# Optimization experiments

Hardware: AMD Instinct MI355X
Metric: run time of the kernel (lower is better)

## Reference

```python
import jax, jax.numpy as jnp
import numpy as np

SERIES_LEN = 4096
D_EMB = 1024
D_V = 1024
HURST = 0.7
H = HURST - 0.5          # exponent used by the module
DT = 1.0 / SERIES_LEN
EPS = 1e-8


def _attn_matrix():
    # Lower-triangular fractional power-law matrix A2[i, j]:
    #   j <  i : ((i - j) * dt + 1e-8) ** (hurst - 0.5)
    #   j == i : 1e-8 ** (hurst - 0.5)
    #   j >  i : 0
    i = jnp.arange(SERIES_LEN, dtype=jnp.int32)[:, None]
    j = jnp.arange(SERIES_LEN, dtype=jnp.int32)[None, :]
    diff = jnp.clip(i - j, 1, None).astype(jnp.float32)  # safe base for fractional power
    lower = jnp.where(i > j, (diff * DT + EPS) ** H, 0.0)
    diag = jnp.eye(SERIES_LEN, dtype=jnp.float32) * (EPS ** H)
    return lower + diag  # (L, L) float32


def setup_inputs() -> dict:
    key = jax.random.key(0)
    k1, k2 = jax.random.split(key)
    embed_series = jax.random.normal(k1, (D_EMB, SERIES_LEN), dtype=jnp.float32)
    # nn.Linear(d_emb, d_v, bias=False) weight has shape (d_v, d_emb)
    Wv_weight = jax.random.normal(k2, (D_V, D_EMB), dtype=jnp.float32) * (1.0 / np.sqrt(D_EMB))
    return {"embed_series": embed_series, "Wv_weight": Wv_weight}


def reference(embed_series, Wv_weight):
    # V (original, d_v x L) = Wv(embed_series.T).T ; output[i, c] = sum_j A2[i, j] * V[c, j]
    # => out = A2 @ (embed_series.T @ Wv_weight.T), shape (L, d_v)
    A2 = _attn_matrix()                                   # (L, L) lower triangular
    Y = jnp.einsum('el,ve->lv', embed_series, Wv_weight)  # (L, d_v)
    return A2 @ Y                                         # (L, d_v)
```

## Files before the change

kernel.cpp:

```cpp
#include <hip/hip_runtime.h>
#include <hip/hip_bf16.h>
#include <cstdint>
#include <cstddef>


#define L_SER 4096
#define DEMB  1024
#define DV    1024

#define R_STRIDE 4224
#define R_O0     4096
#define LDP      72

typedef __bf16 bf16_t;
typedef __attribute__((ext_vector_type(8))) __bf16 bf16x8;
typedef __attribute__((ext_vector_type(4))) float f32x4;

__global__ void prep_kernel(const float* __restrict__ E, const float* __restrict__ W,
                            bf16_t* __restrict__ Eb, bf16_t* __restrict__ Wb,
                            bf16_t* __restrict__ R) {
    const int b = blockIdx.x;
    if (b < 132) {
        int idx = b * 256 + threadIdx.x;
        int s = idx / R_STRIDE;
        int x = idx - s * R_STRIDE;
        int d = R_O0 + s - x;
        float v = 0.0f;
        if (d >= 0 && d < L_SER)
            v = powf((d == 0) ? 1e-8f : ((float)d * (1.0f / (float)L_SER) + 1e-8f), 0.2f);
        R[idx] = (bf16_t)v;
    } else if (b < 132 + 2048) {
        int idx = (b - 132) * 256 + threadIdx.x;
        const f32x4* s = (const f32x4*)E;
        f32x4 v0 = s[idx * 2], v1 = s[idx * 2 + 1];
        bf16x8 o;
        o[0] = (bf16_t)v0[0]; o[1] = (bf16_t)v0[1]; o[2] = (bf16_t)v0[2]; o[3] = (bf16_t)v0[3];
        o[4] = (bf16_t)v1[0]; o[5] = (bf16_t)v1[1]; o[6] = (bf16_t)v1[2]; o[7] = (bf16_t)v1[3];
        ((bf16x8*)Eb)[idx] = o;
    } else {
        int idx = (b - 2180) * 256 + threadIdx.x;
        const f32x4* s = (const f32x4*)W;
        f32x4 v0 = s[idx * 2], v1 = s[idx * 2 + 1];
        bf16x8 o;
        o[0] = (bf16_t)v0[0]; o[1] = (bf16_t)v0[1]; o[2] = (bf16_t)v0[2]; o[3] = (bf16_t)v0[3];
        o[4] = (bf16_t)v1[0]; o[5] = (bf16_t)v1[1]; o[6] = (bf16_t)v1[2]; o[7] = (bf16_t)v1[3];
        ((bf16x8*)Wb)[idx] = o;
    }
}

#define GA_STAGE(SBOFS, RA, RB)                                              \
    _Pragma("unroll")                                                        \
    for (int c = 0; c < 4; ++c) {                                            \
        *(bf16x8*)&sA[(SBOFS) + (c * 32 + srow) * LDP + kc8] = RA[c];        \
        *(bf16x8*)&sB[(SBOFS) + (c * 32 + srow) * LDP + kc8] = RB[c];        \
    }

#define GA_PREFETCH(RA, RB)                                                  \
    _Pragma("unroll")                                                        \
    for (int c = 0; c < 4; ++c) {                                            \
        RA[c] = *(const bf16x8*)pA[c];                                       \
        RB[c] = *(const bf16x8*)pB[c];                                       \
        pA[c] += 64; pB[c] += 64;                                            \
    }

#define GA_COMPUTE(SBOFS)                                                    \
    _Pragma("unroll")                                                        \
    for (int kk = 0; kk < 2; ++kk) {                                         \
        bf16x8 afr[4], bfr[4];                                               \
        _Pragma("unroll")                                                    \
        for (int tm = 0; tm < 4; ++tm)                                       \
            afr[tm] = *(const bf16x8*)&sA[(SBOFS) + (wm * 64 + tm * 16 + ln) * LDP + kk * 32 + quad * 8]; \
        _Pragma("unroll")                                                    \
        for (int tn = 0; tn < 4; ++tn)                                       \
            bfr[tn] = *(const bf16x8*)&sB[(SBOFS) + (wn * 64 + tn * 16 + ln) * LDP + kk * 32 + quad * 8]; \
        _Pragma("unroll")                                                    \
        for (int tm = 0; tm < 4; ++tm)                                       \
            _Pragma("unroll")                                                \
            for (int tn = 0; tn < 4; ++tn)                                   \
                acc[tm][tn] = __builtin_amdgcn_mfma_f32_16x16x32_bf16(afr[tm], bfr[tn], acc[tm][tn], 0, 0, 0); \
    }

__global__ __launch_bounds__(256, 2) void gemm_a_kernel(const bf16_t* __restrict__ R,
                                                        const bf16_t* __restrict__ Eb,
                                                        bf16_t* __restrict__ T0,
                                                        bf16_t* __restrict__ T1) {
    __shared__ __align__(16) bf16_t sA[2 * 128 * LDP];
    __shared__ __align__(16) bf16_t sB[2 * 128 * LDP];

    const int bid = blockIdx.x;
    int I, nb, h;
    if (bid < 256) { I = bid >> 3;                nb = bid & 7;         h = 0; }
    else           { I = 31 - ((bid - 256) >> 3); nb = (bid - 256) & 7; h = 1; }
    const int i0 = I * 128;
    const int n0 = nb * 128;
    const int nsteps = I + 1;
    const int j0b = h ? 64 * (I + 1) : 0;
    bf16_t* __restrict__ Tout = h ? T1 : T0;

    const int tid  = threadIdx.x;
    const int wave = tid >> 6;
    const int lane = tid & 63;
    const int quad = lane >> 4;
    const int ln   = lane & 15;
    const int wm   = wave >> 1;
    const int wn   = wave & 1;
    const int srow = tid >> 3;
    const int kc8  = (tid & 7) * 8;

    f32x4 acc[4][4];
#pragma unroll
    for (int a = 0; a < 4; ++a)
#pragma unroll
        for (int b = 0; b < 4; ++b) acc[a][b] = (f32x4){0, 0, 0, 0};

    const bf16_t* pA[4];
    const bf16_t* pB[4];
    bf16x8 ra0[4], rb0[4], ra1[4], rb1[4];
#pragma unroll
    for (int c = 0; c < 4; ++c) {
        int r = c * 32 + srow;
        pA[c] = R + (size_t)(r & 7) * R_STRIDE + (R_O0 - i0 + j0b - 8 * (r >> 3) + kc8);
        pB[c] = Eb + (size_t)(n0 + c * 32 + srow) * L_SER + j0b + kc8;
    }
    GA_PREFETCH(ra0, rb0)
    if (nsteps > 1) { GA_PREFETCH(ra1, rb1) }

    for (int s = 0;; s += 2) {
        GA_STAGE(0, ra0, rb0)
        __syncthreads();
        if (s + 2 < nsteps) { GA_PREFETCH(ra0, rb0) }
        GA_COMPUTE(0)
        if (s + 1 >= nsteps) break;
        GA_STAGE(128 * LDP, ra1, rb1)
        __syncthreads();
        if (s + 3 < nsteps) { GA_PREFETCH(ra1, rb1) }
        GA_COMPUTE(128 * LDP)
        if (s + 2 >= nsteps) break;
    }

#pragma unroll
    for (int tm = 0; tm < 4; ++tm) {
        int row_base = i0 + wm * 64 + tm * 16 + quad * 4;
#pragma unroll
        for (int tn = 0; tn < 4; ++tn) {
            int col = n0 + wn * 64 + tn * 16 + ln;
#pragma unroll
            for (int r = 0; r < 4; ++r)
                Tout[(size_t)(row_base + r) * DEMB + col] = (bf16_t)acc[tm][tn][r];
        }
    }
}

#define GB_STAGE(SBOFS_A, SBOFS_B, RA, RB)                                   \
    _Pragma("unroll")                                                        \
    for (int c = 0; c < 2; ++c)                                              \
        *(bf16x8*)&sA[(SBOFS_A) + (c * 32 + srow) * LDP + kc8] = RA[c];      \
    _Pragma("unroll")                                                        \
    for (int c = 0; c < 4; ++c)                                              \
        *(bf16x8*)&sB[(SBOFS_B) + (c * 32 + srow) * LDP + kc8] = RB[c];

#define GB_PREFETCH(RA, RB)                                                  \
    _Pragma("unroll")                                                        \
    for (int c = 0; c < 2; ++c) {                                            \
        bf16x8 t0 = *(const bf16x8*)p0[c];                                   \
        bf16x8 t1 = *(const bf16x8*)p1[c];                                   \
        bf16x8 o;                                                            \
        _Pragma("unroll")                                                    \
        for (int u = 0; u < 8; ++u) o[u] = (bf16_t)((float)t0[u] + (float)t1[u]); \
        RA[c] = o;                                                           \
        p0[c] += 64; p1[c] += 64;                                            \
    }                                                                        \
    _Pragma("unroll")                                                        \
    for (int c = 0; c < 4; ++c) {                                            \
        RB[c] = *(const bf16x8*)pW[c];                                       \
        pW[c] += 64;                                                         \
    }

#define GB_COMPUTE(SBOFS_A, SBOFS_B)                                         \
    _Pragma("unroll")                                                        \
    for (int kk = 0; kk < 2; ++kk) {                                         \
        bf16x8 afr[2], bfr[4];                                               \
        _Pragma("unroll")                                                    \
        for (int tm = 0; tm < 2; ++tm)                                       \
            afr[tm] = *(const bf16x8*)&sA[(SBOFS_A) + (wm * 32 + tm * 16 + ln) * LDP + kk * 32 + quad * 8]; \
        _Pragma("unroll")                                                    \
        for (int tn = 0; tn < 4; ++tn)                                       \
            bfr[tn] = *(const bf16x8*)&sB[(SBOFS_B) + (wn * 64 + tn * 16 + ln) * LDP + kk * 32 + quad * 8]; \
        _Pragma("unroll")                                                    \
        for (int tm = 0; tm < 2; ++tm)                                       \
            _Pragma("unroll")                                                \
            for (int tn = 0; tn < 4; ++tn)                                   \
                acc[tm][tn] = __builtin_amdgcn_mfma_f32_16x16x32_bf16(afr[tm], bfr[tn], acc[tm][tn], 0, 0, 0); \
    }

__global__ __launch_bounds__(256, 2) void gemm_b_kernel(const bf16_t* __restrict__ T0,
                                                        const bf16_t* __restrict__ T1,
                                                        const bf16_t* __restrict__ Wb,
                                                        float* __restrict__ out) {
    __shared__ __align__(16) bf16_t sA[2 * 64 * LDP];
    __shared__ __align__(16) bf16_t sB[2 * 128 * LDP];

    const int bid = blockIdx.x;
    const int ib = bid >> 3;
    const int nb = bid & 7;
    const int i0 = ib * 64;
    const int n0 = nb * 128;

    const int tid  = threadIdx.x;
    const int wave = tid >> 6;
    const int lane = tid & 63;
    const int quad = lane >> 4;
    const int ln   = lane & 15;
    const int wm   = wave >> 1;
    const int wn   = wave & 1;
    const int srow = tid >> 3;
    const int kc8  = (tid & 7) * 8;

    f32x4 acc[2][4];
#pragma unroll
    for (int a = 0; a < 2; ++a)
#pragma unroll
        for (int b = 0; b < 4; ++b) acc[a][b] = (f32x4){0, 0, 0, 0};

    const int nsteps = DEMB / 64;

    const bf16_t* p0[2];
    const bf16_t* p1[2];
    const bf16_t* pW[4];
    bf16x8 ra0[2], rb0[4], ra1[2], rb1[4];
#pragma unroll
    for (int c = 0; c < 2; ++c) {
        size_t arow = (size_t)(i0 + c * 32 + srow) * DEMB + kc8;
        p0[c] = T0 + arow;
        p1[c] = T1 + arow;
    }
#pragma unroll
    for (int c = 0; c < 4; ++c)
        pW[c] = Wb + (size_t)(n0 + c * 32 + srow) * DEMB + kc8;

    GB_PREFETCH(ra0, rb0)
    GB_PREFETCH(ra1, rb1)

    for (int s = 0;; s += 2) {
        GB_STAGE(0, 0, ra0, rb0)
        __syncthreads();
        if (s + 2 < nsteps) { GB_PREFETCH(ra0, rb0) }
        GB_COMPUTE(0, 0)
        GB_STAGE(64 * LDP, 128 * LDP, ra1, rb1)
        __syncthreads();
        if (s + 3 < nsteps) { GB_PREFETCH(ra1, rb1) }
        GB_COMPUTE(64 * LDP, 128 * LDP)
        if (s + 2 >= nsteps) break;
    }

#pragma unroll
    for (int tm = 0; tm < 2; ++tm) {
        int row_base = i0 + wm * 32 + tm * 16 + quad * 4;
#pragma unroll
        for (int tn = 0; tn < 4; ++tn) {
            int col = n0 + wn * 64 + tn * 16 + ln;
#pragma unroll
            for (int r = 0; r < 4; ++r)
                out[(size_t)(row_base + r) * DV + col] = acc[tm][tn][r];
        }
    }
}

extern "C" void kernel_launch(void* const* d_in, const int* in_sizes, int n_in,
                              void* d_out, int out_size, void* d_ws, size_t ws_size,
                              hipStream_t stream) {
    const float* E = (const float*)d_in[0];
    const float* W = (const float*)d_in[1];
    float* out = (float*)d_out;

    char* ws = (char*)d_ws;
    bf16_t* Eb = (bf16_t*)(ws);
    bf16_t* T0 = (bf16_t*)(ws + (size_t)8  * 1024 * 1024);
    bf16_t* T1 = (bf16_t*)(ws + (size_t)16 * 1024 * 1024);
    bf16_t* Wb = (bf16_t*)(ws + (size_t)24 * 1024 * 1024);
    bf16_t* R  = (bf16_t*)(ws + (size_t)26 * 1024 * 1024);

    prep_kernel<<<2692, 256, 0, stream>>>(E, W, Eb, Wb, R);
    gemm_a_kernel<<<512, 256, 0, stream>>>(R, Eb, T0, T1);
    gemm_b_kernel<<<512, 256, 0, stream>>>(T0, T1, Wb, out);
}
```

Before: 133.2 us.

## Use direct global-to-LDS loads with XOR-swizzled shared tiles in both GEMMs

Replaces the register-staged prefetch (global load into VGPRs, then ds_write) with the global_load_lds builtin, which writes 16-byte chunks straight into LDS. This is done for both operands of the first GEMM and the W operand of the second. The padded LDS row stride of 72 becomes an unpadded 64 with an XOR chunk swizzle, to avoid bank conflicts without wasting shared memory. The second GEMM's summed T0+T1 operand still goes through registers, but its store now uses the same swizzle. The aim is to cut VGPR pressure and instruction count on the load path. The trade-off is that load latency is hidden only by the double buffer and the wait at each barrier.

New measurement: 125.0 us. -6.1%, faster.

```diff
diff --git a/kernel.cpp b/kernel.cpp
--- a/kernel.cpp
+++ b/kernel.cpp
@@ -10,11 +10,17 @@
 
 #define R_STRIDE 4224
 #define R_O0     4096
-#define LDP      72
 
 typedef __bf16 bf16_t;
 typedef __attribute__((ext_vector_type(8))) __bf16 bf16x8;
 typedef __attribute__((ext_vector_type(4))) float f32x4;
+
+__device__ __forceinline__ void glds16(const bf16_t* g, bf16_t* l) {
+    __builtin_amdgcn_global_load_lds(
+        (const __attribute__((address_space(1))) unsigned int*)(const void*)g,
+        (__attribute__((address_space(3))) unsigned int*)(void*)l,
+        16, 0, 0);
+}
 
 __global__ void prep_kernel(const float* __restrict__ E, const float* __restrict__ W,
                             bf16_t* __restrict__ Eb, bf16_t* __restrict__ Wb,
@@ -48,31 +54,25 @@
     }
 }
 
-#define GA_STAGE(SBOFS, RA, RB)                                              \
+#define GA_STAGE(SBOFS)                                                      \
     _Pragma("unroll")                                                        \
     for (int c = 0; c < 4; ++c) {                                            \
-        *(bf16x8*)&sA[(SBOFS) + (c * 32 + srow) * LDP + kc8] = RA[c];        \
-        *(bf16x8*)&sB[(SBOFS) + (c * 32 + srow) * LDP + kc8] = RB[c];        \
-    }
-
-#define GA_PREFETCH(RA, RB)                                                  \
-    _Pragma("unroll")                                                        \
-    for (int c = 0; c < 4; ++c) {                                            \
-        RA[c] = *(const bf16x8*)pA[c];                                       \
-        RB[c] = *(const bf16x8*)pB[c];                                       \
+        glds16(pA[c], &sA[(SBOFS) + (c * 32 + wave * 8) * 64]);              \
+        glds16(pB[c], &sB[(SBOFS) + (c * 32 + wave * 8) * 64]);              \
         pA[c] += 64; pB[c] += 64;                                            \
     }
 
 #define GA_COMPUTE(SBOFS)                                                    \
     _Pragma("unroll")                                                        \
     for (int kk = 0; kk < 2; ++kk) {                                         \
+        const int co = kk ? coff1 : coff0;                                   \
         bf16x8 afr[4], bfr[4];                                               \
         _Pragma("unroll")                                                    \
         for (int tm = 0; tm < 4; ++tm)                                       \
-            afr[tm] = *(const bf16x8*)&sA[(SBOFS) + (wm * 64 + tm * 16 + ln) * LDP + kk * 32 + quad * 8]; \
+            afr[tm] = *(const bf16x8*)&sA[(SBOFS) + (wm * 64 + tm * 16 + ln) * 64 + co]; \
         _Pragma("unroll")                                                    \
         for (int tn = 0; tn < 4; ++tn)                                       \
-            bfr[tn] = *(const bf16x8*)&sB[(SBOFS) + (wn * 64 + tn * 16 + ln) * LDP + kk * 32 + quad * 8]; \
+            bfr[tn] = *(const bf16x8*)&sB[(SBOFS) + (wn * 64 + tn * 16 + ln) * 64 + co]; \
         _Pragma("unroll")                                                    \
         for (int tm = 0; tm < 4; ++tm)                                       \
             _Pragma("unroll")                                                \
@@ -84,8 +84,8 @@
                                                         const bf16_t* __restrict__ Eb,
                                                         bf16_t* __restrict__ T0,
                                                         bf16_t* __restrict__ T1) {
-    __shared__ __align__(16) bf16_t sA[2 * 128 * LDP];
-    __shared__ __align__(16) bf16_t sB[2 * 128 * LDP];
+    __shared__ __align__(16) bf16_t sA[2 * 128 * 64];
+    __shared__ __align__(16) bf16_t sB[2 * 128 * 64];
 
     const int bid = blockIdx.x;
     int I, nb, h;
@@ -104,8 +104,12 @@
     const int ln   = lane & 15;
     const int wm   = wave >> 1;
     const int wn   = wave & 1;
-    const int srow = tid >> 3;
-    const int kc8  = (tid & 7) * 8;
+
+    const int lrow = lane >> 3;
+    const int lch  = (lane & 7) ^ lrow;
+    const int rsw   = ln & 7;
+    const int coff0 = ((quad ^ rsw)) * 8;
+    const int coff1 = (((4 + quad) ^ rsw)) * 8;
 
     f32x4 acc[4][4];
 #pragma unroll
@@ -115,26 +119,22 @@
 
     const bf16_t* pA[4];
     const bf16_t* pB[4];
-    bf16x8 ra0[4], rb0[4], ra1[4], rb1[4];
 #pragma unroll
     for (int c = 0; c < 4; ++c) {
-        int r = c * 32 + srow;
-        pA[c] = R + (size_t)(r & 7) * R_STRIDE + (R_O0 - i0 + j0b - 8 * (r >> 3) + kc8);
-        pB[c] = Eb + (size_t)(n0 + c * 32 + srow) * L_SER + j0b + kc8;
-    }
-    GA_PREFETCH(ra0, rb0)
-    if (nsteps > 1) { GA_PREFETCH(ra1, rb1) }
-
+        int r = c * 32 + wave * 8 + lrow;
+        pA[c] = R + (size_t)(r & 7) * R_STRIDE + (R_O0 - i0 + j0b - 8 * (r >> 3) + lch * 8);
+        pB[c] = Eb + (size_t)(n0 + r) * L_SER + j0b + lch * 8;
+    }
+
+    GA_STAGE(0)
     for (int s = 0;; s += 2) {
-        GA_STAGE(0, ra0, rb0)
         __syncthreads();
-        if (s + 2 < nsteps) { GA_PREFETCH(ra0, rb0) }
+        if (s + 1 < nsteps) { GA_STAGE(128 * 64) }
         GA_COMPUTE(0)
         if (s + 1 >= nsteps) break;
-        GA_STAGE(128 * LDP, ra1, rb1)
         __syncthreads();
-        if (s + 3 < nsteps) { GA_PREFETCH(ra1, rb1) }
-        GA_COMPUTE(128 * LDP)
+        if (s + 2 < nsteps) { GA_STAGE(0) }
+        GA_COMPUTE(128 * 64)
         if (s + 2 >= nsteps) break;
     }
 
@@ -151,15 +151,12 @@
     }
 }
 
-#define GB_STAGE(SBOFS_A, SBOFS_B, RA, RB)                                   \
+#define GB_STAGE_A(SBOFS, RA)                                                \
     _Pragma("unroll")                                                        \
     for (int c = 0; c < 2; ++c)                                              \
-        *(bf16x8*)&sA[(SBOFS_A) + (c * 32 + srow) * LDP + kc8] = RA[c];      \
-    _Pragma("unroll")                                                        \
-    for (int c = 0; c < 4; ++c)                                              \
-        *(bf16x8*)&sB[(SBOFS_B) + (c * 32 + srow) * LDP + kc8] = RB[c];
-
-#define GB_PREFETCH(RA, RB)                                                  \
+        *(bf16x8*)&sA[(SBOFS) + aofs[c]] = RA[c];
+
+#define GB_LOAD_A(RA)                                                        \
     _Pragma("unroll")                                                        \
     for (int c = 0; c < 2; ++c) {                                            \
         bf16x8 t0 = *(const bf16x8*)p0[c];                                   \
@@ -169,23 +166,26 @@
         for (int u = 0; u < 8; ++u) o[u] = (bf16_t)((float)t0[u] + (float)t1[u]); \
         RA[c] = o;                                                           \
         p0[c] += 64; p1[c] += 64;                                            \
-    }                                                                        \
+    }
+
+#define GB_STAGE_B(SBOFS)                                                    \
     _Pragma("unroll")                                                        \
     for (int c = 0; c < 4; ++c) {                                            \
-        RB[c] = *(const bf16x8*)pW[c];                                       \
+        glds16(pW[c], &sB[(SBOFS) + (c * 32 + wave * 8) * 64]);              \
         pW[c] += 64;                                                         \
     }
 
 #define GB_COMPUTE(SBOFS_A, SBOFS_B)                                         \
     _Pragma("unroll")                                                        \
     for (int kk = 0; kk < 2; ++kk) {                                         \
+        const int co = kk ? coff1 : coff0;                                   \
         bf16x8 afr[2], bfr[4];                                               \
         _Pragma("unroll")                                                    \
         for (int tm = 0; tm < 2; ++tm)                                       \
-            afr[tm] = *(const bf16x8*)&sA[(SBOFS_A) + (wm * 32 + tm * 16 + ln) * LDP + kk * 32 + quad * 8]; \
+            afr[tm] = *(const bf16x8*)&sA[(SBOFS_A) + (wm * 32 + tm * 16 + ln) * 64 + co]; \
         _Pragma("unroll")                                                    \
         for (int tn = 0; tn < 4; ++tn)                                       \
-            bfr[tn] = *(const bf16x8*)&sB[(SBOFS_B) + (wn * 64 + tn * 16 + ln) * LDP + kk * 32 + quad * 8]; \
+            bfr[tn] = *(const bf16x8*)&sB[(SBOFS_B) + (wn * 64 + tn * 16 + ln) * 64 + co]; \
         _Pragma("unroll")                                                    \
         for (int tm = 0; tm < 2; ++tm)                                       \
             _Pragma("unroll")                                                \
@@ -197,8 +197,8 @@
                                                         const bf16_t* __restrict__ T1,
                                                         const bf16_t* __restrict__ Wb,
                                                         float* __restrict__ out) {
-    __shared__ __align__(16) bf16_t sA[2 * 64 * LDP];
-    __shared__ __align__(16) bf16_t sB[2 * 128 * LDP];
+    __shared__ __align__(16) bf16_t sA[2 * 64 * 64];
+    __shared__ __align__(16) bf16_t sB[2 * 128 * 64];
 
     const int bid = blockIdx.x;
     const int ib = bid >> 3;
@@ -214,7 +214,18 @@
     const int wm   = wave >> 1;
     const int wn   = wave & 1;
     const int srow = tid >> 3;
-    const int kc8  = (tid & 7) * 8;
+    const int t8   = tid & 7;
+
+    const int lrow = lane >> 3;
+    const int lch  = (lane & 7) ^ lrow;
+    const int rsw   = ln & 7;
+    const int coff0 = ((quad ^ rsw)) * 8;
+    const int coff1 = (((4 + quad) ^ rsw)) * 8;
+
+    int aofs[2];
+#pragma unroll
+    for (int c = 0; c < 2; ++c)
+        aofs[c] = (c * 32 + srow) * 64 + (t8 ^ (srow & 7)) * 8;
 
     f32x4 acc[2][4];
 #pragma unroll
@@ -227,29 +238,32 @@
     const bf16_t* p0[2];
     const bf16_t* p1[2];
     const bf16_t* pW[4];
-    bf16x8 ra0[2], rb0[4], ra1[2], rb1[4];
+    bf16x8 ra0[2], ra1[2];
 #pragma unroll
     for (int c = 0; c < 2; ++c) {
-        size_t arow = (size_t)(i0 + c * 32 + srow) * DEMB + kc8;
+        size_t arow = (size_t)(i0 + c * 32 + srow) * DEMB + t8 * 8;
         p0[c] = T0 + arow;
         p1[c] = T1 + arow;
     }
 #pragma unroll
     for (int c = 0; c < 4; ++c)
-        pW[c] = Wb + (size_t)(n0 + c * 32 + srow) * DEMB + kc8;
-
-    GB_PREFETCH(ra0, rb0)
-    GB_PREFETCH(ra1, rb1)
+        pW[c] = Wb + (size_t)(n0 + c * 32 + wave * 8 + lrow) * DEMB + lch * 8;
+
+    GB_LOAD_A(ra0)
+    GB_LOAD_A(ra1)
+    GB_STAGE_B(0)
 
     for (int s = 0;; s += 2) {
-        GB_STAGE(0, 0, ra0, rb0)
+        GB_STAGE_A(0, ra0)
         __syncthreads();
-        if (s + 2 < nsteps) { GB_PREFETCH(ra0, rb0) }
+        if (s + 2 < nsteps) { GB_LOAD_A(ra0) }
+        if (s + 1 < nsteps) { GB_STAGE_B(128 * 64) }
         GB_COMPUTE(0, 0)
-        GB_STAGE(64 * LDP, 128 * LDP, ra1, rb1)
+        GB_STAGE_A(64 * 64, ra1)
         __syncthreads();
-        if (s + 3 < nsteps) { GB_PREFETCH(ra1, rb1) }
-        GB_COMPUTE(64 * LDP, 128 * LDP)
+        if (s + 3 < nsteps) { GB_LOAD_A(ra1) }
+        if (s + 2 < nsteps) { GB_STAGE_B(0) }
+        GB_COMPUTE(64 * 64, 128 * 64)
         if (s + 2 >= nsteps) break;
     }
 
```
